# Kernel optimization log

Measured on AMD Instinct MI355X. Metric: run time of the kernel, lower is better.

Reference implementation:

```python
import jax, jax.numpy as jnp
import numpy as np

D_MODEL = 1024
BATCH, SEQ = 4, 4096


def setup_inputs() -> dict:
    key = jax.random.key(0)
    ks = jax.random.split(key, 4)
    scale = 1.0 / np.sqrt(D_MODEL)  # lecun_normal-ish init for Dense kernels
    x = jax.random.normal(ks[0], (BATCH, SEQ, D_MODEL), dtype=jnp.float32)
    Wf = jax.random.normal(ks[1], (D_MODEL, D_MODEL), dtype=jnp.float32) * scale
    Wi = jax.random.normal(ks[2], (D_MODEL, D_MODEL), dtype=jnp.float32) * scale
    Wb = jax.random.normal(ks[3], (D_MODEL, D_MODEL), dtype=jnp.float32) * scale
    bf = jnp.full((D_MODEL,), -4.0, dtype=jnp.float32)  # forget bias -> f~0.018
    bi = jnp.full((D_MODEL,), 4.0, dtype=jnp.float32)   # input bias  -> i~0.982
    bb = jnp.zeros((D_MODEL,), dtype=jnp.float32)
    return {"x": x, "Wf": Wf, "bf": bf, "Wi": Wi, "bi": bi, "Wb": Wb, "bb": bb}


def _scan_combine(c1, c2):
    a1, b1 = c1
    a2, b2 = c2
    # linear recurrence composition: h = a2*(a1*h_prev + b1) + b2
    return a1 * a2, a2 * b1 + b2


def reference(x, Wf, bf, Wi, bi, Wb, bb):
    # gates + drive: [B, S, D]
    f = jax.nn.sigmoid(jnp.einsum('bsd,de->bse', x, Wf) + bf)
    i = jax.nn.sigmoid(jnp.einsum('bsd,de->bse', x, Wi) + bi)
    b = (jnp.einsum('bsd,de->bse', x, Wb) + bb) / jnp.sqrt(jnp.float32(x.shape[-1]))
    a = (1.0 - f).astype(jnp.complex64)
    b_gated = (i * b).astype(jnp.complex64)
    # parallel associative scan over time axis: h_t = a_t * h_{t-1} + b_t
    _, state = jax.lax.associative_scan(_scan_combine, (a, b_gated), axis=1)
    return state.real
```

## Files before the change

### kernel.cpp

```cpp
#include <hip/hip_runtime.h>
#include <cstdint>

#define D_MODEL 1024
#define BATCH 4
#define SEQ 4096
#define M_TOT (BATCH*SEQ)

#define BM 256
#define BNG 64
#define BK 64
#define NKT (D_MODEL/BK)

#define XS_BYTES (BM*BK*2)
#define WG_BYTES (BNG*BK*2)
#define TILE_BYTES (XS_BYTES + 3*WG_BYTES)
#define SMEM_BYTES (2*TILE_BYTES)

#define NCHUNK 64
#define CHUNK 64

typedef __bf16 bf16x8 __attribute__((ext_vector_type(8)));
typedef float f32x4 __attribute__((ext_vector_type(4)));
typedef unsigned short u16x8 __attribute__((ext_vector_type(8)));

static __device__ __forceinline__ unsigned short f2bf(float f) {
    unsigned int u = __float_as_uint(f);
    return (unsigned short)((u + 0x7fffu + ((u >> 16) & 1u)) >> 16);
}
static __device__ __forceinline__ float ubf(unsigned short u) {
    return __uint_as_float((unsigned int)u << 16);
}

__global__ void k_convert_x(const float* __restrict__ x, unsigned short* __restrict__ xb) {
    int i = blockIdx.x * 256 + threadIdx.x;
    const float4* p = (const float4*)x;
    float4 v0 = p[2*i], v1 = p[2*i+1];
    u16x8 r;
    r[0] = f2bf(v0.x); r[1] = f2bf(v0.y); r[2] = f2bf(v0.z); r[3] = f2bf(v0.w);
    r[4] = f2bf(v1.x); r[5] = f2bf(v1.y); r[6] = f2bf(v1.z); r[7] = f2bf(v1.w);
    *(u16x8*)(xb + (size_t)i * 8) = r;
}

__global__ void k_transpose_w(const float* __restrict__ Wf, const float* __restrict__ Wi,
                              const float* __restrict__ Wb, unsigned short* __restrict__ wt) {
    __shared__ float tile[32][33];
    int g = blockIdx.z;
    const float* W = (g == 0) ? Wf : (g == 1) ? Wi : Wb;
    int n0 = blockIdx.x * 32, k0 = blockIdx.y * 32;
    int tx = threadIdx.x, ty = threadIdx.y;
    for (int j = 0; j < 4; ++j)
        tile[ty + j*8][tx] = W[(size_t)(k0 + ty + j*8) * D_MODEL + n0 + tx];
    __syncthreads();
    for (int j = 0; j < 4; ++j) {
        int n = n0 + ty + j*8;
        wt[(size_t)g * D_MODEL * D_MODEL + (size_t)n * D_MODEL + k0 + tx] = f2bf(tile[tx][ty + j*8]);
    }
}

#define GL16(gp, lp) \
    __builtin_amdgcn_global_load_lds((const __attribute__((address_space(1))) void*)(gp), \
                                     (__attribute__((address_space(3))) void*)(lp), 16, 0, 0)

__launch_bounds__(512)
__global__ void k_gemm_gates(const unsigned short* __restrict__ xb, const unsigned short* __restrict__ wt,
                             const float* __restrict__ bfv, const float* __restrict__ biv,
                             const float* __restrict__ bbv,
                             unsigned short* __restrict__ f_out, unsigned short* __restrict__ bg_out,
                             float* __restrict__ Ac, float* __restrict__ Bc) {
    extern __shared__ char smem[];
    const int tid  = threadIdx.x;
    const int wave = tid >> 6;
    const int lane = tid & 63;
    const int lr = lane & 15, lg = lane >> 4;
    const int bid = blockIdx.x;
    const int swz = (bid & 7) * 128 + (bid >> 3);
    const int mb = swz >> 4;
    const int nb = swz & 15;
    const int m0 = mb * BM;
    const int n0 = nb * BNG;
    const int wr = wave >> 2;
    const int wc = wave & 3;
    const int wrow = wr * 128;

    const int srow = tid >> 3;
    const int scb  = ((tid & 7) * 16) ^ ((srow & 7) << 4);
    const unsigned short* sA0 = xb + (size_t)(m0 +   0 + srow) * D_MODEL + (scb >> 1);
    const unsigned short* sA1 = xb + (size_t)(m0 +  64 + srow) * D_MODEL + (scb >> 1);
    const unsigned short* sA2 = xb + (size_t)(m0 + 128 + srow) * D_MODEL + (scb >> 1);
    const unsigned short* sA3 = xb + (size_t)(m0 + 192 + srow) * D_MODEL + (scb >> 1);
    const unsigned short* sB0 = wt + 0ull*D_MODEL*D_MODEL + (size_t)(n0 + srow) * D_MODEL + (scb >> 1);
    const unsigned short* sB1 = wt + 1ull*D_MODEL*D_MODEL + (size_t)(n0 + srow) * D_MODEL + (scb >> 1);
    const unsigned short* sB2 = wt + 2ull*D_MODEL*D_MODEL + (size_t)(n0 + srow) * D_MODEL + (scb >> 1);

#define STAGE_A(db) do { char* _d = smem + (db)*TILE_BYTES + wave*1024; \
        GL16(sA0, _d + 0*8192); GL16(sA1, _d + 1*8192); \
        GL16(sA2, _d + 2*8192); GL16(sA3, _d + 3*8192); \
        sA0 += BK; sA1 += BK; sA2 += BK; sA3 += BK; } while (0)
#define STAGE_B01(db) do { char* _d = smem + (db)*TILE_BYTES + XS_BYTES + wave*1024; \
        GL16(sB0, _d + 0*8192); GL16(sB1, _d + 1*8192); \
        sB0 += BK; sB1 += BK; } while (0)
#define STAGE_B2(db) do { char* _d = smem + (db)*TILE_BYTES + XS_BYTES + 2*8192 + wave*1024; \
        GL16(sB2, _d); sB2 += BK; } while (0)

    f32x4 acc[3][8] = {};
    const int sxor = (lr & 7) << 4;

    STAGE_A(0); STAGE_B01(0); STAGE_B2(0);
    asm volatile("s_waitcnt vmcnt(1)" ::: "memory");
    __builtin_amdgcn_s_barrier();

    bf16x8 af[2][4], af2[2][4], bw01[2][2], bw2[2];

#define READS_P1(tb) do { _Pragma("unroll") for (int kk = 0; kk < 2; ++kk) { \
        const int ko = (kk*64 + lg*16) ^ sxor; \
        _Pragma("unroll") for (int mi = 0; mi < 4; ++mi) \
            af[kk][mi] = *(const bf16x8*)((tb) + (wrow + mi*16 + lr)*128 + ko); \
        _Pragma("unroll") for (int g = 0; g < 2; ++g) \
            bw01[kk][g] = *(const bf16x8*)((tb) + XS_BYTES + g*WG_BYTES + (wc*16 + lr)*128 + ko); } } while (0)
#define READS_P2(tb) do { _Pragma("unroll") for (int kk = 0; kk < 2; ++kk) { \
        const int ko = (kk*64 + lg*16) ^ sxor; \
        _Pragma("unroll") for (int mi = 0; mi < 4; ++mi) \
            af2[kk][mi] = *(const bf16x8*)((tb) + (wrow + (mi+4)*16 + lr)*128 + ko); } } while (0)
#define READS_P3(tb) do { _Pragma("unroll") for (int kk = 0; kk < 2; ++kk) { \
        const int ko = (kk*64 + lg*16) ^ sxor; \
        bw2[kk] = *(const bf16x8*)((tb) + XS_BYTES + 2*WG_BYTES + (wc*16 + lr)*128 + ko); } } while (0)
#define MFMA_P1 do { _Pragma("unroll") for (int g = 0; g < 2; ++g) \
        _Pragma("unroll") for (int mi = 0; mi < 4; ++mi) \
        _Pragma("unroll") for (int kk = 0; kk < 2; ++kk) \
            acc[g][mi] = __builtin_amdgcn_mfma_f32_16x16x32_bf16(af[kk][mi], bw01[kk][g], acc[g][mi], 0,0,0); } while (0)
#define MFMA_P2 do { _Pragma("unroll") for (int g = 0; g < 2; ++g) \
        _Pragma("unroll") for (int mi = 0; mi < 4; ++mi) \
        _Pragma("unroll") for (int kk = 0; kk < 2; ++kk) \
            acc[g][mi+4] = __builtin_amdgcn_mfma_f32_16x16x32_bf16(af2[kk][mi], bw01[kk][g], acc[g][mi+4], 0,0,0); } while (0)
#define MFMA_P3 do { _Pragma("unroll") for (int mi = 0; mi < 4; ++mi) \
        _Pragma("unroll") for (int kk = 0; kk < 2; ++kk) { \
            acc[2][mi]   = __builtin_amdgcn_mfma_f32_16x16x32_bf16(af[kk][mi],  bw2[kk], acc[2][mi],   0,0,0); \
            acc[2][mi+4] = __builtin_amdgcn_mfma_f32_16x16x32_bf16(af2[kk][mi], bw2[kk], acc[2][mi+4], 0,0,0); } } while (0)
#define LGKM_FENCE do { asm volatile("s_waitcnt lgkmcnt(0)" ::: "memory"); \
        __builtin_amdgcn_sched_barrier(0); } while (0)

    #pragma unroll 1
    for (int kt = 0; kt < NKT - 1; ++kt) {
        const char* tb = smem + (kt & 1) * TILE_BYTES;
        const int db = (kt + 1) & 1;
        READS_P1(tb);
        STAGE_A(db);
        __builtin_amdgcn_s_barrier();
        LGKM_FENCE;
        __builtin_amdgcn_s_setprio(1); MFMA_P1; __builtin_amdgcn_s_setprio(0);
        __builtin_amdgcn_s_barrier();
        READS_P2(tb);
        STAGE_B01(db);
        asm volatile("s_waitcnt vmcnt(6)" ::: "memory");
        __builtin_amdgcn_s_barrier();
        LGKM_FENCE;
        __builtin_amdgcn_s_setprio(1); MFMA_P2; __builtin_amdgcn_s_setprio(0);
        __builtin_amdgcn_s_barrier();
        READS_P3(tb);
        STAGE_B2(db);
        asm volatile("s_waitcnt vmcnt(1)" ::: "memory");
        __builtin_amdgcn_s_barrier();
        LGKM_FENCE;
        __builtin_amdgcn_s_setprio(1); MFMA_P3; __builtin_amdgcn_s_setprio(0);
        __builtin_amdgcn_s_barrier();
    }
    {
        const char* tb = smem + ((NKT - 1) & 1) * TILE_BYTES;
        READS_P1(tb);
        __builtin_amdgcn_s_barrier();
        LGKM_FENCE;
        __builtin_amdgcn_s_setprio(1); MFMA_P1; __builtin_amdgcn_s_setprio(0);
        __builtin_amdgcn_s_barrier();
        READS_P2(tb);
        asm volatile("s_waitcnt vmcnt(0)" ::: "memory");
        __builtin_amdgcn_s_barrier();
        LGKM_FENCE;
        __builtin_amdgcn_s_setprio(1); MFMA_P2; __builtin_amdgcn_s_setprio(0);
        __builtin_amdgcn_s_barrier();
        READS_P3(tb);
        LGKM_FENCE;
        __builtin_amdgcn_s_setprio(1); MFMA_P3; __builtin_amdgcn_s_setprio(0);
    }

    {
        const int col = n0 + wc*16 + lr;
        const float vbf = bfv[col], vbi = biv[col], vbb = bbv[col];
        float sA[2][4], sB[2][4];
        #pragma unroll
        for (int mi = 0; mi < 8; ++mi) {
            float Ap = 1.0f, Bp = 0.0f;
            #pragma unroll
            for (int r = 0; r < 4; ++r) {
                const int row = m0 + wrow + mi*16 + lg*4 + r;
                const float zf = acc[0][mi][r] + vbf;
                const float zi = acc[1][mi][r] + vbi;
                const float zb = (acc[2][mi][r] + vbb) * 0.03125f;
                const float fg = 1.0f / (1.0f + __expf(-zf));
                const float ig = 1.0f / (1.0f + __expf(-zi));
                const unsigned short fu  = f2bf(fg);
                const unsigned short bgu = f2bf(ig * zb);
                const float a_r  = 1.0f - ubf(fu);
                const float bg_r = ubf(bgu);
                const size_t o = (size_t)row * D_MODEL + col;
                f_out[o]  = fu;
                bg_out[o] = bgu;
                Bp = fmaf(a_r, Bp, bg_r);
                Ap *= a_r;
            }
            sA[mi >> 2][mi & 3] = Ap;
            sB[mi >> 2][mi & 3] = Bp;
        }
        #pragma unroll
        for (int half = 0; half < 2; ++half) {
            float CA = 1.0f, CB = 0.0f;
            #pragma unroll
            for (int q = 0; q < 4; ++q) {
                float A = sA[half][q], B = sB[half][q];
                float Ao = __shfl_xor(A, 16), Bo = __shfl_xor(B, 16);
                float B1 = (lg & 1) ? fmaf(A, Bo, B) : fmaf(Ao, B, Bo);
                float A1 = A * Ao;
                Ao = __shfl_xor(A1, 32); Bo = __shfl_xor(B1, 32);
                float B2 = (lg & 2) ? fmaf(A1, Bo, B1) : fmaf(Ao, B1, Bo);
                float A2 = A1 * Ao;
                CB = fmaf(A2, CB, B2);
                CA = CA * A2;
            }
            if (lg == 0) {
                const int chG = mb * 4 + wr * 2 + half;
                Ac[(size_t)chG * D_MODEL + col] = CA;
                Bc[(size_t)chG * D_MODEL + col] = CB;
            }
        }
    }
}

__global__ void k_chunk_prefix(const float* __restrict__ Ac, const float* __restrict__ Bc,
                               float* __restrict__ H) {
    const int d = (blockIdx.x & 3) * 256 + threadIdx.x;
    const int b = blockIdx.x >> 2;
    float h = 0.0f;
    for (int c = 0; c < NCHUNK; ++c) {
        const size_t o = ((size_t)b * NCHUNK + c) * D_MODEL + d;
        H[o] = h;
        h = fmaf(Ac[o], h, Bc[o]);
    }
}

__global__ void k_apply(const unsigned short* __restrict__ f, const unsigned short* __restrict__ bg,
                        const float* __restrict__ H, float* __restrict__ out) {
    const int d0 = (blockIdx.x & 1) * 512 + threadIdx.x * 2;
    const int c = (blockIdx.x >> 1) & 63;
    const int b = blockIdx.x >> 7;
    const size_t base = ((size_t)b * SEQ + (size_t)c * CHUNK) * D_MODEL + d0;
    const size_t hoff = ((size_t)b * NCHUNK + c) * D_MODEL + d0;
    float h0 = H[hoff], h1 = H[hoff + 1];
    for (int t = 0; t < CHUNK; ++t) {
        const size_t o = base + (size_t)t * D_MODEL;
        const unsigned int fv = *(const unsigned int*)(f + o);
        const unsigned int gv = *(const unsigned int*)(bg + o);
        const float a0 = 1.0f - __uint_as_float(fv << 16);
        const float a1 = 1.0f - __uint_as_float(fv & 0xffff0000u);
        const float b0 = __uint_as_float(gv << 16);
        const float b1 = __uint_as_float(gv & 0xffff0000u);
        h0 = fmaf(a0, h0, b0);
        h1 = fmaf(a1, h1, b1);
        *(float2*)(out + o) = make_float2(h0, h1);
    }
}

extern "C" void kernel_launch(void* const* d_in, const int* in_sizes, int n_in,
                              void* d_out, int out_size, void* d_ws, size_t ws_size,
                              hipStream_t stream) {
    const float* x   = (const float*)d_in[0];
    const float* Wf  = (const float*)d_in[1];
    const float* bfv = (const float*)d_in[2];
    const float* Wi  = (const float*)d_in[3];
    const float* biv = (const float*)d_in[4];
    const float* Wb  = (const float*)d_in[5];
    const float* bbv = (const float*)d_in[6];
    float* out = (float*)d_out;

    char* ws = (char*)d_ws;
    unsigned short* fbuf  = (unsigned short*)ws;
    unsigned short* bgbuf = (unsigned short*)(ws + (32ull << 20));
    unsigned short* xb    = (unsigned short*)(ws + (64ull << 20));
    unsigned short* wt    = (unsigned short*)(ws + (96ull << 20));
    float* Ac = (float*)(ws + (102ull << 20));
    float* Bc = (float*)(ws + (103ull << 20));
    float* Hb = (float*)(ws + (64ull << 20));

    hipFuncSetAttribute((const void*)k_gemm_gates,
                        hipFuncAttributeMaxDynamicSharedMemorySize, SMEM_BYTES);

    hipLaunchKernelGGL(k_convert_x, dim3((M_TOT * D_MODEL / 8) / 256), dim3(256), 0, stream, x, xb);
    hipLaunchKernelGGL(k_transpose_w, dim3(32, 32, 3), dim3(32, 8), 0, stream, Wf, Wi, Wb, wt);
    hipLaunchKernelGGL(k_gemm_gates, dim3((M_TOT / BM) * (D_MODEL / BNG)), dim3(512), SMEM_BYTES, stream,
                       xb, wt, bfv, biv, bbv, fbuf, bgbuf, Ac, Bc);
    hipLaunchKernelGGL(k_chunk_prefix, dim3(BATCH * (D_MODEL / 256)), dim3(256), 0, stream,
                       Ac, Bc, Hb);
    hipLaunchKernelGGL(k_apply, dim3(BATCH * NCHUNK * 2), dim3(256), 0, stream,
                       fbuf, bgbuf, Hb, out);
}
```

Baseline: 168.4 us.

## Replace phased GEMM main loop with simple double-buffered compute loop

```diff
diff --git a/kernel.cpp b/kernel.cpp
--- a/kernel.cpp
+++ b/kernel.cpp
@@ -92,94 +92,66 @@
     const unsigned short* sB1 = wt + 1ull*D_MODEL*D_MODEL + (size_t)(n0 + srow) * D_MODEL + (scb >> 1);
     const unsigned short* sB2 = wt + 2ull*D_MODEL*D_MODEL + (size_t)(n0 + srow) * D_MODEL + (scb >> 1);
 
-#define STAGE_A(db) do { char* _d = smem + (db)*TILE_BYTES + wave*1024; \
+#define STAGE(db) do { \
+        char* _d = smem + (db)*TILE_BYTES + wave*1024; \
         GL16(sA0, _d + 0*8192); GL16(sA1, _d + 1*8192); \
         GL16(sA2, _d + 2*8192); GL16(sA3, _d + 3*8192); \
-        sA0 += BK; sA1 += BK; sA2 += BK; sA3 += BK; } while (0)
-#define STAGE_B01(db) do { char* _d = smem + (db)*TILE_BYTES + XS_BYTES + wave*1024; \
-        GL16(sB0, _d + 0*8192); GL16(sB1, _d + 1*8192); \
-        sB0 += BK; sB1 += BK; } while (0)
-#define STAGE_B2(db) do { char* _d = smem + (db)*TILE_BYTES + XS_BYTES + 2*8192 + wave*1024; \
-        GL16(sB2, _d); sB2 += BK; } while (0)
+        char* _e = _d + XS_BYTES; \
+        GL16(sB0, _e + 0*8192); GL16(sB1, _e + 1*8192); GL16(sB2, _e + 2*8192); \
+        sA0 += BK; sA1 += BK; sA2 += BK; sA3 += BK; \
+        sB0 += BK; sB1 += BK; sB2 += BK; \
+    } while (0)
 
     f32x4 acc[3][8] = {};
     const int sxor = (lr & 7) << 4;
 
-    STAGE_A(0); STAGE_B01(0); STAGE_B2(0);
-    asm volatile("s_waitcnt vmcnt(1)" ::: "memory");
-    __builtin_amdgcn_s_barrier();
-
-    bf16x8 af[2][4], af2[2][4], bw01[2][2], bw2[2];
-
-#define READS_P1(tb) do { _Pragma("unroll") for (int kk = 0; kk < 2; ++kk) { \
-        const int ko = (kk*64 + lg*16) ^ sxor; \
-        _Pragma("unroll") for (int mi = 0; mi < 4; ++mi) \
-            af[kk][mi] = *(const bf16x8*)((tb) + (wrow + mi*16 + lr)*128 + ko); \
-        _Pragma("unroll") for (int g = 0; g < 2; ++g) \
-            bw01[kk][g] = *(const bf16x8*)((tb) + XS_BYTES + g*WG_BYTES + (wc*16 + lr)*128 + ko); } } while (0)
-#define READS_P2(tb) do { _Pragma("unroll") for (int kk = 0; kk < 2; ++kk) { \
-        const int ko = (kk*64 + lg*16) ^ sxor; \
-        _Pragma("unroll") for (int mi = 0; mi < 4; ++mi) \
-            af2[kk][mi] = *(const bf16x8*)((tb) + (wrow + (mi+4)*16 + lr)*128 + ko); } } while (0)
-#define READS_P3(tb) do { _Pragma("unroll") for (int kk = 0; kk < 2; ++kk) { \
-        const int ko = (kk*64 + lg*16) ^ sxor; \
-        bw2[kk] = *(const bf16x8*)((tb) + XS_BYTES + 2*WG_BYTES + (wc*16 + lr)*128 + ko); } } while (0)
-#define MFMA_P1 do { _Pragma("unroll") for (int g = 0; g < 2; ++g) \
-        _Pragma("unroll") for (int mi = 0; mi < 4; ++mi) \
-        _Pragma("unroll") for (int kk = 0; kk < 2; ++kk) \
-            acc[g][mi] = __builtin_amdgcn_mfma_f32_16x16x32_bf16(af[kk][mi], bw01[kk][g], acc[g][mi], 0,0,0); } while (0)
-#define MFMA_P2 do { _Pragma("unroll") for (int g = 0; g < 2; ++g) \
-        _Pragma("unroll") for (int mi = 0; mi < 4; ++mi) \
-        _Pragma("unroll") for (int kk = 0; kk < 2; ++kk) \
-            acc[g][mi+4] = __builtin_amdgcn_mfma_f32_16x16x32_bf16(af2[kk][mi], bw01[kk][g], acc[g][mi+4], 0,0,0); } while (0)
-#define MFMA_P3 do { _Pragma("unroll") for (int mi = 0; mi < 4; ++mi) \
-        _Pragma("unroll") for (int kk = 0; kk < 2; ++kk) { \
-            acc[2][mi]   = __builtin_amdgcn_mfma_f32_16x16x32_bf16(af[kk][mi],  bw2[kk], acc[2][mi],   0,0,0); \
-            acc[2][mi+4] = __builtin_amdgcn_mfma_f32_16x16x32_bf16(af2[kk][mi], bw2[kk], acc[2][mi+4], 0,0,0); } } while (0)
-#define LGKM_FENCE do { asm volatile("s_waitcnt lgkmcnt(0)" ::: "memory"); \
-        __builtin_amdgcn_sched_barrier(0); } while (0)
-
-    #pragma unroll 1
-    for (int kt = 0; kt < NKT - 1; ++kt) {
+    STAGE(0);
+    __syncthreads();
+
+    for (int kt = 0; kt < NKT; ++kt) {
+        if (kt + 1 < NKT) STAGE((kt + 1) & 1);
         const char* tb = smem + (kt & 1) * TILE_BYTES;
-        const int db = (kt + 1) & 1;
-        READS_P1(tb);
-        STAGE_A(db);
-        __builtin_amdgcn_s_barrier();
-        LGKM_FENCE;
-        __builtin_amdgcn_s_setprio(1); MFMA_P1; __builtin_amdgcn_s_setprio(0);
-        __builtin_amdgcn_s_barrier();
-        READS_P2(tb);
-        STAGE_B01(db);
-        asm volatile("s_waitcnt vmcnt(6)" ::: "memory");
-        __builtin_amdgcn_s_barrier();
-        LGKM_FENCE;
-        __builtin_amdgcn_s_setprio(1); MFMA_P2; __builtin_amdgcn_s_setprio(0);
-        __builtin_amdgcn_s_barrier();
-        READS_P3(tb);
-        STAGE_B2(db);
-        asm volatile("s_waitcnt vmcnt(1)" ::: "memory");
-        __builtin_amdgcn_s_barrier();
-        LGKM_FENCE;
-        __builtin_amdgcn_s_setprio(1); MFMA_P3; __builtin_amdgcn_s_setprio(0);
-        __builtin_amdgcn_s_barrier();
-    }
-    {
-        const char* tb = smem + ((NKT - 1) & 1) * TILE_BYTES;
-        READS_P1(tb);
-        __builtin_amdgcn_s_barrier();
-        LGKM_FENCE;
-        __builtin_amdgcn_s_setprio(1); MFMA_P1; __builtin_amdgcn_s_setprio(0);
-        __builtin_amdgcn_s_barrier();
-        READS_P2(tb);
-        asm volatile("s_waitcnt vmcnt(0)" ::: "memory");
-        __builtin_amdgcn_s_barrier();
-        LGKM_FENCE;
-        __builtin_amdgcn_s_setprio(1); MFMA_P2; __builtin_amdgcn_s_setprio(0);
-        __builtin_amdgcn_s_barrier();
-        READS_P3(tb);
-        LGKM_FENCE;
-        __builtin_amdgcn_s_setprio(1); MFMA_P3; __builtin_amdgcn_s_setprio(0);
+        #pragma unroll
+        for (int kk = 0; kk < 2; ++kk) {
+            const int ko = (kk*64 + lg*16) ^ sxor;
+            const int bro = (wc*16 + lr)*128 + ko;
+            bf16x8 bw0 = *(const bf16x8*)(tb + XS_BYTES + 0*WG_BYTES + bro);
+            bf16x8 bw1 = *(const bf16x8*)(tb + XS_BYTES + 1*WG_BYTES + bro);
+            bf16x8 bw2 = *(const bf16x8*)(tb + XS_BYTES + 2*WG_BYTES + bro);
+            bf16x8 a0 = *(const bf16x8*)(tb + (wrow + 0*16 + lr)*128 + ko);
+            bf16x8 a1 = *(const bf16x8*)(tb + (wrow + 1*16 + lr)*128 + ko);
+            bf16x8 a2 = *(const bf16x8*)(tb + (wrow + 2*16 + lr)*128 + ko);
+            bf16x8 a3 = *(const bf16x8*)(tb + (wrow + 3*16 + lr)*128 + ko);
+            acc[0][0] = __builtin_amdgcn_mfma_f32_16x16x32_bf16(a0, bw0, acc[0][0], 0,0,0);
+            acc[1][0] = __builtin_amdgcn_mfma_f32_16x16x32_bf16(a0, bw1, acc[1][0], 0,0,0);
+            acc[2][0] = __builtin_amdgcn_mfma_f32_16x16x32_bf16(a0, bw2, acc[2][0], 0,0,0);
+            acc[0][1] = __builtin_amdgcn_mfma_f32_16x16x32_bf16(a1, bw0, acc[0][1], 0,0,0);
+            acc[1][1] = __builtin_amdgcn_mfma_f32_16x16x32_bf16(a1, bw1, acc[1][1], 0,0,0);
+            acc[2][1] = __builtin_amdgcn_mfma_f32_16x16x32_bf16(a1, bw2, acc[2][1], 0,0,0);
+            acc[0][2] = __builtin_amdgcn_mfma_f32_16x16x32_bf16(a2, bw0, acc[0][2], 0,0,0);
+            acc[1][2] = __builtin_amdgcn_mfma_f32_16x16x32_bf16(a2, bw1, acc[1][2], 0,0,0);
+            acc[2][2] = __builtin_amdgcn_mfma_f32_16x16x32_bf16(a2, bw2, acc[2][2], 0,0,0);
+            acc[0][3] = __builtin_amdgcn_mfma_f32_16x16x32_bf16(a3, bw0, acc[0][3], 0,0,0);
+            acc[1][3] = __builtin_amdgcn_mfma_f32_16x16x32_bf16(a3, bw1, acc[1][3], 0,0,0);
+            acc[2][3] = __builtin_amdgcn_mfma_f32_16x16x32_bf16(a3, bw2, acc[2][3], 0,0,0);
+            bf16x8 a4 = *(const bf16x8*)(tb + (wrow + 4*16 + lr)*128 + ko);
+            bf16x8 a5 = *(const bf16x8*)(tb + (wrow + 5*16 + lr)*128 + ko);
+            bf16x8 a6 = *(const bf16x8*)(tb + (wrow + 6*16 + lr)*128 + ko);
+            bf16x8 a7 = *(const bf16x8*)(tb + (wrow + 7*16 + lr)*128 + ko);
+            acc[0][4] = __builtin_amdgcn_mfma_f32_16x16x32_bf16(a4, bw0, acc[0][4], 0,0,0);
+            acc[1][4] = __builtin_amdgcn_mfma_f32_16x16x32_bf16(a4, bw1, acc[1][4], 0,0,0);
+            acc[2][4] = __builtin_amdgcn_mfma_f32_16x16x32_bf16(a4, bw2, acc[2][4], 0,0,0);
+            acc[0][5] = __builtin_amdgcn_mfma_f32_16x16x32_bf16(a5, bw0, acc[0][5], 0,0,0);
+            acc[1][5] = __builtin_amdgcn_mfma_f32_16x16x32_bf16(a5, bw1, acc[1][5], 0,0,0);
+            acc[2][5] = __builtin_amdgcn_mfma_f32_16x16x32_bf16(a5, bw2, acc[2][5], 0,0,0);
+            acc[0][6] = __builtin_amdgcn_mfma_f32_16x16x32_bf16(a6, bw0, acc[0][6], 0,0,0);
+            acc[1][6] = __builtin_amdgcn_mfma_f32_16x16x32_bf16(a6, bw1, acc[1][6], 0,0,0);
+            acc[2][6] = __builtin_amdgcn_mfma_f32_16x16x32_bf16(a6, bw2, acc[2][6], 0,0,0);
+            acc[0][7] = __builtin_amdgcn_mfma_f32_16x16x32_bf16(a7, bw0, acc[0][7], 0,0,0);
+            acc[1][7] = __builtin_amdgcn_mfma_f32_16x16x32_bf16(a7, bw1, acc[1][7], 0,0,0);
+            acc[2][7] = __builtin_amdgcn_mfma_f32_16x16x32_bf16(a7, bw2, acc[2][7], 0,0,0);
+        }
+        __syncthreads();
     }
 
     {
@@ -232,6 +204,7 @@
             }
         }
     }
+#undef STAGE
 }
 
 __global__ void k_chunk_prefix(const float* __restrict__ Ac, const float* __restrict__ Bc,
```

Result: no change. 167.8 us (-0.4%).
